# Optimization experiments

Hardware: AMD Instinct MI355X
Metric: run time of the kernel (lower is better)

The kernel has to match this reference:

```python
import jax, jax.numpy as jnp
import numpy as np
from jax import lax

C_CLIP = 10.0
TEMP = 1.0
NEG = 1e8


def setup_inputs() -> dict:
    key = jax.random.key(0)
    ks = jax.random.split(key, 20)
    B, N, H, M = 16, 1000, 128, 2
    s = 0.08
    inp = {
        "enc_h": jax.random.normal(ks[0], (B, N, H), jnp.float32),
        "mask0": jnp.zeros((B, N), jnp.float32),
        "Wq1": jax.random.normal(ks[1], (M, 2 * H, H), jnp.float32) * s,
        "Wref1": jax.random.normal(ks[2], (M, H, H), jnp.float32) * s,
        "Vec1": jax.random.normal(ks[3], (M, H, H), jnp.float32) * s,
        "Wq3": jax.random.normal(ks[4], (M, H, H), jnp.float32) * s,
        "Wref3": jax.random.normal(ks[5], (M, H, H), jnp.float32) * s,
        "Vec3": jax.random.normal(ks[6], (M, H, H), jnp.float32) * s,
        "Wq4": jax.random.normal(ks[7], (M, H, H), jnp.float32) * s,
        "Wref4": jax.random.normal(ks[8], (M, H, H), jnp.float32) * s,
        "Vec4": jax.random.normal(ks[9], (M, H, H), jnp.float32) * s,
        "Wmh": jax.random.normal(ks[10], (M * H, H), jnp.float32) * s,
        "Wq2": jax.random.normal(ks[11], (H, H), jnp.float32) * s,
        "Wref2": jax.random.normal(ks[12], (H, H), jnp.float32) * s,
        "Vec2": jax.random.normal(ks[13], (H,), jnp.float32) * s,
        "dec_inp": jax.random.normal(ks[14], (H,), jnp.float32) * s,
        "n_decode": 16,
    }
    return inp


def reference(enc_h, mask0, Wq1, Wref1, Vec1, Wq3, Wref3, Vec3,
              Wq4, Wref4, Vec4, Wmh, Wq2, Wref2, Vec2, dec_inp, n_decode):
    B, N, H = enc_h.shape
    ref = enc_h
    h_mean = ref.mean(axis=1)  # [B,H] graph embedding (encoder mean)
    # Precompute per-head reference projections (hoisted out of decode loop)
    r1 = jnp.einsum('bnd,mdh->bmnh', ref, Wref1)
    v1 = jnp.einsum('bnd,mdh->bmnh', ref, Vec1)
    r3 = jnp.einsum('bnd,mdh->bmnh', ref, Wref3)
    v3 = jnp.einsum('bnd,mdh->bmnh', ref, Vec3)
    r4 = jnp.einsum('bnd,mdh->bmnh', ref, Wref4)
    v4 = jnp.einsum('bnd,mdh->bmnh', ref, Vec4)
    r2 = ref @ Wref2  # [B,N,H]

    def glimpse(query, Wq, r, v, mask):
        # query: [B,Din]; r,v: [B,M,N,H]; mask: [B,N] (1 = unavailable)
        q = jnp.einsum('bi,mih->bmh', query, Wq)
        u = jnp.tanh(q[:, :, None, :] + r)              # [B,M,N,H]
        s = jnp.einsum('bmnh,bmnh->bmn', u, v)          # additive scores
        s = C_CLIP * jnp.tanh(s)                        # logit clipping
        s = s - NEG * mask[:, None, :]
        a = jax.nn.softmax(s, axis=-1)                  # [B,M,N]
        g = jnp.einsum('bmn,bmnh->bmh', a, r)           # per-head glimpse
        return g.reshape(B, -1) @ Wmh                   # merge heads -> [B,H]

    def step(carry, _):
        mask, prev = carry
        q0 = jnp.concatenate([h_mean, prev], axis=-1)   # [B,2H]
        q = glimpse(q0, Wq1, r1, v1, mask)
        q = glimpse(q, Wq3, r3, v3, mask)
        q = glimpse(q, Wq4, r4, v4, mask)
        # pointer logits: Vec2 . tanh(W_q2 q + W_ref2 ref)
        u = jnp.einsum('h,bnh->bn', Vec2, jnp.tanh((q @ Wq2)[:, None, :] + r2))
        u = C_CLIP * jnp.tanh(u)
        u = u - NEG * mask
        logp = jax.nn.log_softmax(u / TEMP, axis=-1)    # [B,N]
        sel = jnp.argmax(logp, axis=-1)                 # greedy job selection
        mask = mask.at[jnp.arange(B), sel].set(1.0)
        prev = jnp.take_along_axis(ref, sel[:, None, None], axis=1)[:, 0]
        return (mask, prev), (logp, sel)

    prev0 = jnp.broadcast_to(dec_inp, (B, H))
    (_, _), (logps, sels) = lax.scan(step, (mask0, prev0), None, length=n_decode)
    return logps, sels
```

## Files before the change

### kernel.cpp

```cpp
#include <hip/hip_runtime.h>


#define Bb 16
#define Nn 1000
#define Hh 128
#define Ss 16
#define TPB 1024
#define NW 16
#define NB 16
#define ROWS 63
#define TPT (Nn * Bb * Hh)

#define PPART(par, g, c, m) \
  ((((size_t)(par)*16 + (size_t)(g))*NB + (size_t)(c))*2 + (size_t)(m))*132
#define ABUF(buf, g) (((size_t)(buf)*16 + (size_t)(g)) * 272)

typedef float f32x4 __attribute__((ext_vector_type(4)));
#define NTL(p) __builtin_nontemporal_load((const f32x4*)(p))

__device__ __forceinline__ void red5_2(float& a, float& b) {
#pragma unroll
  for (int m = 1; m <= 16; m <<= 1) {
    a += __shfl_xor(a, m, 64);
    b += __shfl_xor(b, m, 64);
  }
}
__device__ __forceinline__ void red5_4(float& a, float& b, float& c, float& d) {
#pragma unroll
  for (int m = 1; m <= 16; m <<= 1) {
    a += __shfl_xor(a, m, 64);
    b += __shfl_xor(b, m, 64);
    c += __shfl_xor(c, m, 64);
    d += __shfl_xor(d, m, 64);
  }
}

__device__ __forceinline__ float tanh_fast(float x) {
  const float xc = fminf(fmaxf(x, -10.f), 10.f);
  const float e = __expf(xc + xc);
  return (e - 1.f) * __builtin_amdgcn_rcpf(e + 1.f);
}
__device__ __forceinline__ float dot4t(const f32x4 q, const f32x4 r, const f32x4 v) {
  return tanh_fast(q[0] + r[0]) * v[0] + tanh_fast(q[1] + r[1]) * v[1] +
         tanh_fast(q[2] + r[2]) * v[2] + tanh_fast(q[3] + r[3]) * v[3];
}

__device__ __forceinline__ float aload(const float* p) {
  return __hip_atomic_load(p, __ATOMIC_RELAXED, __HIP_MEMORY_SCOPE_AGENT);
}
__device__ __forceinline__ void astore(float* p, float v) {
  __hip_atomic_store(p, v, __ATOMIC_RELAXED, __HIP_MEMORY_SCOPE_AGENT);
}

__device__ __forceinline__ void gbar(int* fl, int c, int p, int tid, int lane) {
  __syncthreads();
  if (tid < 64) {
    if (lane == 0)
      __hip_atomic_store(&fl[c * 32], p, __ATOMIC_RELEASE, __HIP_MEMORY_SCOPE_AGENT);
    int v = p;
    while (true) {
      if (lane < NB)
        v = __hip_atomic_load(&fl[lane * 32], __ATOMIC_RELAXED, __HIP_MEMORY_SCOPE_AGENT);
      if (__all(v >= p)) break;
    }
  }
  __syncthreads();
}

__global__ __launch_bounds__(256) void ptr1_proj_kernel(
    const float* __restrict__ enc,
    const float* __restrict__ Wref1, const float* __restrict__ Vec1,
    const float* __restrict__ Wref3, const float* __restrict__ Vec3,
    const float* __restrict__ Wref4, const float* __restrict__ Vec4,
    const float* __restrict__ Wref2,
    float* __restrict__ outp) {
  __shared__ float At[128][64];
  __shared__ float Bs[128][64];
  const int rt = blockIdx.x;
  const int wy = blockIdx.y;
  const int mat = wy >> 1;
  const int ch = wy & 1;
  const int tid = threadIdx.x;

  const float* W;
  switch (mat >> 1) {
    case 0: W = Wref1; break;
    case 1: W = Vec1;  break;
    case 2: W = Wref3; break;
    case 3: W = Vec3;  break;
    case 4: W = Wref4; break;
    case 5: W = Vec4;  break;
    default: W = Wref2; break;
  }
  if (mat < 12) W += (size_t)(mat & 1) * (128 * 128);

  const float* asrc = enc + (size_t)rt * 64 * 128;
  for (int f = tid; f < 64 * 32; f += 256) {
    const int r = f >> 5, k4 = (f & 31) << 2;
    const float4 v = *(const float4*)(asrc + (size_t)r * 128 + k4);
    At[k4 + 0][r] = v.x; At[k4 + 1][r] = v.y;
    At[k4 + 2][r] = v.z; At[k4 + 3][r] = v.w;
  }
  for (int f = tid; f < 128 * 16; f += 256) {
    const int k = f >> 4, c4 = (f & 15) << 2;
    *(float4*)&Bs[k][c4] = *(const float4*)(W + (size_t)k * 128 + ch * 64 + c4);
  }
  __syncthreads();

  const int tx = tid & 15, ty = tid >> 4;
  float acc[4][4] = {{0.f}};
  for (int k = 0; k < 128; ++k) {
    const float4 a = *(const float4*)&At[k][ty * 4];
    const float4 b = *(const float4*)&Bs[k][tx * 4];
    acc[0][0] += a.x * b.x; acc[0][1] += a.x * b.y; acc[0][2] += a.x * b.z; acc[0][3] += a.x * b.w;
    acc[1][0] += a.y * b.x; acc[1][1] += a.y * b.y; acc[1][2] += a.y * b.z; acc[1][3] += a.y * b.w;
    acc[2][0] += a.z * b.x; acc[2][1] += a.z * b.y; acc[2][2] += a.z * b.z; acc[2][3] += a.z * b.w;
    acc[3][0] += a.w * b.x; acc[3][1] += a.w * b.y; acc[3][2] += a.w * b.z; acc[3][3] += a.w * b.w;
  }
  float* dst = outp + (size_t)mat * TPT + ((size_t)rt * 64 + ty * 4) * 128 + ch * 64 + tx * 4;
  for (int i = 0; i < 4; ++i) {
    float4 v; v.x = acc[i][0]; v.y = acc[i][1]; v.z = acc[i][2]; v.w = acc[i][3];
    *(float4*)(dst + (size_t)i * 128) = v;
  }
}

__global__ __launch_bounds__(1024, 4) void ptr1_decode_kernel(
    const float* __restrict__ enc, const float* __restrict__ mask0,
    const float* __restrict__ Wq1, const float* __restrict__ Wq3,
    const float* __restrict__ Wq4, const float* __restrict__ Wmh,
    const float* __restrict__ Wq2, const float* __restrict__ Vec2,
    const float* __restrict__ dec_inp, const float* __restrict__ proj,
    float* __restrict__ partials, float* __restrict__ accum,
    int* __restrict__ flags, float* __restrict__ out) {
  const int g = blockIdx.x >> 4;
  const int c = blockIdx.x & 15;
  const int tid = threadIdx.x;
  const int wv = tid >> 6;
  const int lane = tid & 63;
  const int half = lane >> 5;
  const int hl = lane & 31;
  const int h0 = hl << 2;
  const int start = c * ROWS;
  const int cnt = min(ROWS, Nn - start);
  const int jrow = wv * 2 + half;
  const int j2 = jrow + 32;
  const bool a2 = j2 < cnt;
  const int j2c = a2 ? j2 : jrow;
  int* fl = flags + g * (16 * 32);

  __shared__ float Wmh_lds[256 * 128];
  __shared__ __align__(16) float hmean[128];
  __shared__ __align__(16) float qprev[128];
  __shared__ __align__(16) float qcur[128];
  __shared__ __align__(16) float base1[256];
  __shared__ __align__(16) float qm[2][128];
  __shared__ __align__(16) float gfraw[256];
  __shared__ __align__(16) float vecl[128];
  __shared__ __align__(16) float wpart[NW][2][132];
  __shared__ __align__(16) float qpart[4][256];
  __shared__ __align__(16) float mpart[8][128];
  __shared__ float sS[2];
  __shared__ float maskl[64];
  __shared__ float ulocal[64];
  __shared__ int sel_sh;
  __shared__ float logZ_sh;

  {
    float4* wl = (float4*)Wmh_lds;
    const float4* wg = (const float4*)Wmh;
#pragma unroll
    for (int k = 0; k < 8; ++k) wl[tid + k * TPB] = wg[tid + k * TPB];
  }
  if (tid < 128) vecl[tid] = Vec2[tid];
  for (int j = tid; j < cnt; j += TPB) maskl[j] = mask0[(size_t)g * Nn + start + j];

  const size_t o1 = (size_t)jrow * Hh;
  const size_t o2 = (size_t)j2c * Hh;

  {
    const float* eb = enc + ((size_t)g * Nn + start) * Hh + h0;
    const float4 eA = *(const float4*)(eb + o1);
    const float4 eB = *(const float4*)(eb + o2);
    float4 a;
    a.x = eA.x + (a2 ? eB.x : 0.f); a.y = eA.y + (a2 ? eB.y : 0.f);
    a.z = eA.z + (a2 ? eB.z : 0.f); a.w = eA.w + (a2 ? eB.w : 0.f);
    a.x += __shfl_xor(a.x, 32, 64); a.y += __shfl_xor(a.y, 32, 64);
    a.z += __shfl_xor(a.z, 32, 64); a.w += __shfl_xor(a.w, 32, 64);
    if (half == 0) *(float4*)&wpart[wv][0][4 + h0] = a;
    __syncthreads();
    if (tid < 128) {
      float s = 0.f;
      for (int w = 0; w < NW; ++w) s += wpart[w][0][4 + tid];
      astore(&partials[PPART(0, g, c, 0) + 4 + tid], s);
    }
    gbar(fl, c, 1, tid, lane);
    if (tid < 128) {
      float s = 0.f;
#pragma unroll 8
      for (int cc = 0; cc < NB; ++cc) s += aload(&partials[PPART(0, g, cc, 0) + 4 + tid]);
      hmean[tid] = s * (1.0f / (float)Nn);
    }
    if (tid >= 128 && tid < 256) qprev[tid - 128] = dec_inp[tid - 128];
    __syncthreads();
    {
      const int o = tid & 255, part = tid >> 8;
      const int m = o >> 7, h = o & 127;
      const float* wp = Wq1 + (size_t)m * 256 * 128 + (size_t)(part * 32) * 128 + h;
      const float* qc = hmean + part * 32;
      float acc = 0.f;
#pragma unroll 16
      for (int i = 0; i < 32; ++i) acc += qc[i] * wp[(size_t)i * 128];
      qpart[part][o] = acc;
    }
    __syncthreads();
    if (tid < 256)
      base1[tid] = qpart[0][tid] + qpart[1][tid] + qpart[2][tid] + qpart[3][tid];
    __syncthreads();
  }

  int p = 2;
  for (int step = 0; step < Ss; ++step) {
    for (int gl = 0; gl < 3; ++gl) {
      const size_t rowb = ((size_t)g * Nn + start) * Hh + h0;
      const float* r0p = proj + (size_t)(4 * gl + 0) * TPT + rowb;
      const float* r1p = proj + (size_t)(4 * gl + 1) * TPT + rowb;
      const float* v0p = proj + (size_t)(4 * gl + 2) * TPT + rowb;
      const float* v1p = proj + (size_t)(4 * gl + 3) * TPT + rowb;
      const f32x4 r0A = NTL(r0p + o1), r0B = NTL(r0p + o2);
      const f32x4 r1A = NTL(r1p + o1), r1B = NTL(r1p + o2);
      const f32x4 v0A = NTL(v0p + o1), v0B = NTL(v0p + o2);
      const f32x4 v1A = NTL(v1p + o1), v1B = NTL(v1p + o2);
      __builtin_amdgcn_sched_barrier(0);
      {
        const int o = tid & 255, part = tid >> 8;
        const int m = o >> 7, h = o & 127;
        const float* wp;
        const float* qc;
        if (gl == 0) {
          wp = Wq1 + (size_t)m * 256 * 128 + (size_t)(128 + part * 32) * 128 + h;
          qc = qprev + part * 32;
        } else {
          const float* Wq = (gl == 1) ? Wq3 : Wq4;
          wp = Wq + (size_t)m * 128 * 128 + (size_t)(part * 32) * 128 + h;
          qc = qcur + part * 32;
        }
        float acc = 0.f;
#pragma unroll 16
        for (int i = 0; i < 32; ++i) acc += qc[i] * wp[(size_t)i * 128];
        qpart[part][o] = acc;
      }
      __syncthreads();
      if (tid < 256) {
        float s = qpart[0][tid] + qpart[1][tid] + qpart[2][tid] + qpart[3][tid];
        if (gl == 0) s += base1[tid];
        (&qm[0][0])[tid] = s;
      }
      __syncthreads();

      const f32x4 qa = *(const f32x4*)&qm[0][h0];
      const f32x4 qb = *(const f32x4*)&qm[1][h0];
      const float mlA = maskl[jrow], mlB = maskl[j2c];
      float s0A = dot4t(qa, r0A, v0A), s1A = dot4t(qb, r1A, v1A);
      float s0B = dot4t(qa, r0B, v0B), s1B = dot4t(qb, r1B, v1B);
      red5_4(s0A, s1A, s0B, s1B);
      s0A = 10.f * tanh_fast(s0A) - 1e8f * mlA;
      s1A = 10.f * tanh_fast(s1A) - 1e8f * mlA;
      s0B = 10.f * tanh_fast(s0B) - 1e8f * mlB;
      s1B = 10.f * tanh_fast(s1B) - 1e8f * mlB;
      const float e0A = __expf(s0A - 10.f), e1A = __expf(s1A - 10.f);
      const float e0B = a2 ? __expf(s0B - 10.f) : 0.f;
      const float e1B = a2 ? __expf(s1B - 10.f) : 0.f;
      float S0 = e0A + e0B, S1 = e1A + e1B;
      float4 g0, g1;
      g0.x = e0A * r0A[0] + e0B * r0B[0]; g0.y = e0A * r0A[1] + e0B * r0B[1];
      g0.z = e0A * r0A[2] + e0B * r0B[2]; g0.w = e0A * r0A[3] + e0B * r0B[3];
      g1.x = e1A * r1A[0] + e1B * r1B[0]; g1.y = e1A * r1A[1] + e1B * r1B[1];
      g1.z = e1A * r1A[2] + e1B * r1B[2]; g1.w = e1A * r1A[3] + e1B * r1B[3];
      S0 += __shfl_xor(S0, 32, 64); S1 += __shfl_xor(S1, 32, 64);
      g0.x += __shfl_xor(g0.x, 32, 64); g0.y += __shfl_xor(g0.y, 32, 64);
      g0.z += __shfl_xor(g0.z, 32, 64); g0.w += __shfl_xor(g0.w, 32, 64);
      g1.x += __shfl_xor(g1.x, 32, 64); g1.y += __shfl_xor(g1.y, 32, 64);
      g1.z += __shfl_xor(g1.z, 32, 64); g1.w += __shfl_xor(g1.w, 32, 64);
      if (half == 0) {
        *(float4*)&wpart[wv][0][4 + h0] = g0;
        *(float4*)&wpart[wv][1][4 + h0] = g1;
        if (hl == 0) { wpart[wv][0][0] = S0; wpart[wv][1][0] = S1; }
      }
      __syncthreads();
      float* ab = accum + ABUF(p & 3, g);
      float* zb = accum + ABUF((p + 1) & 3, g);
      if (tid < 256) {
        const int m = tid >> 7, h = tid & 127;
        float gs = 0.f;
        for (int w = 0; w < NW; ++w) gs += wpart[w][m][4 + h];
        unsafeAtomicAdd(&ab[m * 132 + 4 + h], gs);
        if (h == 0) {
          float ss = 0.f;
          for (int w = 0; w < NW; ++w) ss += wpart[w][m][0];
          unsafeAtomicAdd(&ab[m * 132], ss);
        }
      } else if (tid >= 512 && tid < 512 + 17) {
        const int idx = c * 17 + (tid - 512);
        if (idx < 272) astore(&zb[idx], 0.f);
      }
      gbar(fl, c, p, tid, lane);
      p++;
      if (tid < 256) gfraw[tid] = aload(&ab[(tid >> 7) * 132 + 4 + (tid & 127)]);
      if (tid >= 256 && tid < 258) sS[tid - 256] = aload(&ab[(tid - 256) * 132]);
      __syncthreads();
      {
        const int h = tid & 127, part = tid >> 7;
        const int m = part >> 2;
        float acc = 0.f;
        const float* wl = Wmh_lds + (size_t)part * 32 * 128 + h;
        const float* gg = gfraw + part * 32;
#pragma unroll 16
        for (int i = 0; i < 32; ++i) acc += gg[i] * wl[i * 128];
        mpart[part][h] = acc / sS[m];
      }
      __syncthreads();
      if (tid < 128) {
        float acc = 0.f;
        for (int w = 0; w < 8; ++w) acc += mpart[w][tid];
        qcur[tid] = acc;
      }
      __syncthreads();
    }

    const float* r2p = proj + (size_t)12 * TPT + ((size_t)g * Nn + start) * Hh + h0;
    const f32x4 rrA = NTL(r2p + o1);
    const f32x4 rrB = NTL(r2p + o2);
    __builtin_amdgcn_sched_barrier(0);
    {
      const int h = tid & 127, part = tid >> 7;
      float acc = 0.f;
      const float* wp = Wq2 + (size_t)part * 16 * 128 + h;
      const float* qc = qcur + part * 16;
#pragma unroll
      for (int i = 0; i < 16; ++i) acc += qc[i] * wp[(size_t)i * 128];
      mpart[part][h] = acc;
    }
    __syncthreads();
    if (tid < 128) {
      float acc = 0.f;
      for (int w = 0; w < 8; ++w) acc += mpart[w][tid];
      qm[0][tid] = acc;
    }
    __syncthreads();
    {
      const f32x4 q2 = *(const f32x4*)&qm[0][h0];
      const f32x4 vz = *(const f32x4*)&vecl[h0];
      float upA = dot4t(q2, rrA, vz);
      float upB = dot4t(q2, rrB, vz);
      red5_2(upA, upB);
      const float mlA = maskl[jrow], mlB = maskl[j2c];
      const float uA = 10.f * tanh_fast(upA) - 1e8f * mlA;
      const float uB = a2 ? (10.f * tanh_fast(upB) - 1e8f * mlB) : -3.0e38f;
      if (hl == 0) {
        ulocal[jrow] = uA;
        if (a2) ulocal[j2] = uB;
      }
      float Sv = __expf(uA - 10.f) + (a2 ? __expf(uB - 10.f) : 0.f);
      float um = uA; int ui = start + jrow;
      if (a2 && uB > um) { um = uB; ui = start + j2; }
      Sv += __shfl_xor(Sv, 32, 64);
      const float um2 = __shfl_xor(um, 32, 64);
      const int ui2 = __shfl_xor(ui, 32, 64);
      if (um2 > um || (um2 == um && ui2 < ui)) { um = um2; ui = ui2; }
      if (lane == 0) {
        wpart[wv][0][0] = Sv; wpart[wv][0][1] = um;
        wpart[wv][0][2] = __int_as_float(ui);
      }
    }
    __syncthreads();
    float* ab = accum + ABUF(p & 3, g);
    float* zb = accum + ABUF((p + 1) & 3, g);
    if (tid == 0) {
      float St = 0.f, bm = -3.0e38f; int bi = 0x7fffffff;
      for (int ww = 0; ww < NW; ++ww) {
        St += wpart[ww][0][0];
        const float m2 = wpart[ww][0][1];
        const int i2 = __float_as_int(wpart[ww][0][2]);
        if (m2 > bm || (m2 == bm && i2 < bi)) { bm = m2; bi = i2; }
      }
      unsigned ob = __float_as_uint(bm);
      ob = (ob & 0x80000000u) ? ~ob : (ob | 0x80000000u);
      const unsigned long long key =
          ((unsigned long long)ob << 32) | (0xFFFFFFFFu - (unsigned)bi);
      unsafeAtomicAdd(&ab[0], St);
      atomicMax((unsigned long long*)&ab[264], key);
    } else if (tid >= 512 && tid < 512 + 17) {
      const int idx = c * 17 + (tid - 512);
      if (idx < 272) astore(&zb[idx], 0.f);
    }
    gbar(fl, c, p, tid, lane);
    p++;
    if (tid == 0) {
      const float St = aload(&ab[0]);
      const unsigned long long key = __hip_atomic_load(
          (const unsigned long long*)&ab[264], __ATOMIC_RELAXED,
          __HIP_MEMORY_SCOPE_AGENT);
      sel_sh = (int)(0xFFFFFFFFu - (unsigned)(key & 0xFFFFFFFFu));
      logZ_sh = 10.f + __logf(St);
    }
    __syncthreads();
    const int sel = sel_sh;
    const float lz = logZ_sh;
    if (tid < 128)
      qprev[tid] = enc[((size_t)g * Nn + sel) * Hh + tid];
    for (int j = tid; j < cnt; j += TPB)
      out[(size_t)step * (Bb * Nn) + (size_t)g * Nn + start + j] = ulocal[j] - lz;
    if (c == 0 && tid == 0)
      out[(size_t)Ss * Bb * Nn + (size_t)step * Bb + g] = (float)sel;
    if (tid == 0 && sel >= start && sel < start + cnt) maskl[sel - start] = 1.0f;
    __syncthreads();
  }
}

extern "C" void kernel_launch(void* const* d_in, const int* in_sizes, int n_in,
                              void* d_out, int out_size, void* d_ws, size_t ws_size,
                              hipStream_t stream) {
  const float* enc     = (const float*)d_in[0];
  const float* mask0   = (const float*)d_in[1];
  const float* Wq1     = (const float*)d_in[2];
  const float* Wref1   = (const float*)d_in[3];
  const float* Vec1    = (const float*)d_in[4];
  const float* Wq3     = (const float*)d_in[5];
  const float* Wref3   = (const float*)d_in[6];
  const float* Vec3    = (const float*)d_in[7];
  const float* Wq4     = (const float*)d_in[8];
  const float* Wref4   = (const float*)d_in[9];
  const float* Vec4    = (const float*)d_in[10];
  const float* Wmh     = (const float*)d_in[11];
  const float* Wq2     = (const float*)d_in[12];
  const float* Wref2   = (const float*)d_in[13];
  const float* Vec2    = (const float*)d_in[14];
  const float* dec_inp = (const float*)d_in[15];
  float* out = (float*)d_out;

  char* ws = (char*)d_ws;
  int* flags      = (int*)ws;
  float* accum    = (float*)(ws + 32768);
  float* partials = (float*)(ws + 102400);
  float* proj     = (float*)(ws + 102400 + 540672);

  hipMemsetAsync(ws, 0, 102400, stream);

  dim3 pg(250, 26);
  ptr1_proj_kernel<<<pg, 256, 0, stream>>>(enc, Wref1, Vec1, Wref3, Vec3,
                                           Wref4, Vec4, Wref2, proj);

  void* args[] = {(void*)&enc,  (void*)&mask0, (void*)&Wq1, (void*)&Wq3,
                  (void*)&Wq4,  (void*)&Wmh,   (void*)&Wq2, (void*)&Vec2,
                  (void*)&dec_inp, (void*)&proj, (void*)&partials,
                  (void*)&accum, (void*)&flags, (void*)&out};
  hipLaunchCooperativeKernel((const void*)ptr1_decode_kernel, dim3(256),
                             dim3(1024), args, 0, stream);
}
```

Measured before the change: 993.9 us.

## Keep projection tiles in registers across decode steps and merge heads before barrier

Loads all 13 per-row projection tiles (r/v for three glimpses plus r2) into registers once before the decode loop, instead of re-reading them from global memory on every step. The per-block glimpse partials are pushed through the Wmh head-merge before the grid barrier, so each block atomically adds merged 128-wide vectors and the post-barrier work is a cheap normalize. Launch bounds are relaxed to 2 blocks per CU to allow the extra register use. This risks register pressure or spills, and the reordered sums change floating-point rounding.

```diff
diff --git a/kernel.cpp b/kernel.cpp
--- a/kernel.cpp
+++ b/kernel.cpp
@@ -11,8 +11,7 @@
 #define ROWS 63
 #define TPT (Nn * Bb * Hh)
 
-#define PPART(par, g, c, m) \
-  ((((size_t)(par)*16 + (size_t)(g))*NB + (size_t)(c))*2 + (size_t)(m))*132
+#define PPART(g, c) (((size_t)(g)*NB + (size_t)(c)) * 132)
 #define ABUF(buf, g) (((size_t)(buf)*16 + (size_t)(g)) * 272)
 
 typedef float f32x4 __attribute__((ext_vector_type(4)));
@@ -124,7 +123,7 @@
   }
 }
 
-__global__ __launch_bounds__(1024, 4) void ptr1_decode_kernel(
+__global__ __launch_bounds__(1024, 2) void ptr1_decode_kernel(
     const float* __restrict__ enc, const float* __restrict__ mask0,
     const float* __restrict__ Wq1, const float* __restrict__ Wq3,
     const float* __restrict__ Wq4, const float* __restrict__ Wmh,
@@ -159,11 +158,29 @@
   __shared__ __align__(16) float wpart[NW][2][132];
   __shared__ __align__(16) float qpart[4][256];
   __shared__ __align__(16) float mpart[8][128];
-  __shared__ float sS[2];
   __shared__ float maskl[64];
   __shared__ float ulocal[64];
   __shared__ int sel_sh;
   __shared__ float logZ_sh;
+
+  const size_t o1 = (size_t)jrow * Hh;
+  const size_t o2 = (size_t)j2c * Hh;
+  const size_t rowb = ((size_t)g * Nn + start) * Hh + h0;
+  const float* pb = proj + rowb;
+
+  const f32x4 G0r0A = NTL(pb + (size_t)0 * TPT + o1), G0r0B = NTL(pb + (size_t)0 * TPT + o2);
+  const f32x4 G0r1A = NTL(pb + (size_t)1 * TPT + o1), G0r1B = NTL(pb + (size_t)1 * TPT + o2);
+  const f32x4 G0v0A = NTL(pb + (size_t)2 * TPT + o1), G0v0B = NTL(pb + (size_t)2 * TPT + o2);
+  const f32x4 G0v1A = NTL(pb + (size_t)3 * TPT + o1), G0v1B = NTL(pb + (size_t)3 * TPT + o2);
+  const f32x4 G1r0A = NTL(pb + (size_t)4 * TPT + o1), G1r0B = NTL(pb + (size_t)4 * TPT + o2);
+  const f32x4 G1r1A = NTL(pb + (size_t)5 * TPT + o1), G1r1B = NTL(pb + (size_t)5 * TPT + o2);
+  const f32x4 G1v0A = NTL(pb + (size_t)6 * TPT + o1), G1v0B = NTL(pb + (size_t)6 * TPT + o2);
+  const f32x4 G1v1A = NTL(pb + (size_t)7 * TPT + o1), G1v1B = NTL(pb + (size_t)7 * TPT + o2);
+  const f32x4 G2r0A = NTL(pb + (size_t)8 * TPT + o1), G2r0B = NTL(pb + (size_t)8 * TPT + o2);
+  const f32x4 G2r1A = NTL(pb + (size_t)9 * TPT + o1), G2r1B = NTL(pb + (size_t)9 * TPT + o2);
+  const f32x4 G2v0A = NTL(pb + (size_t)10 * TPT + o1), G2v0B = NTL(pb + (size_t)10 * TPT + o2);
+  const f32x4 G2v1A = NTL(pb + (size_t)11 * TPT + o1), G2v1B = NTL(pb + (size_t)11 * TPT + o2);
+  const f32x4 rrA  = NTL(pb + (size_t)12 * TPT + o1), rrB  = NTL(pb + (size_t)12 * TPT + o2);
 
   {
     float4* wl = (float4*)Wmh_lds;
@@ -174,11 +191,8 @@
   if (tid < 128) vecl[tid] = Vec2[tid];
   for (int j = tid; j < cnt; j += TPB) maskl[j] = mask0[(size_t)g * Nn + start + j];
 
-  const size_t o1 = (size_t)jrow * Hh;
-  const size_t o2 = (size_t)j2c * Hh;
-
   {
-    const float* eb = enc + ((size_t)g * Nn + start) * Hh + h0;
+    const float* eb = enc + rowb;
     const float4 eA = *(const float4*)(eb + o1);
     const float4 eB = *(const float4*)(eb + o2);
     float4 a;
@@ -191,13 +205,13 @@
     if (tid < 128) {
       float s = 0.f;
       for (int w = 0; w < NW; ++w) s += wpart[w][0][4 + tid];
-      astore(&partials[PPART(0, g, c, 0) + 4 + tid], s);
+      astore(&partials[PPART(g, c) + 4 + tid], s);
     }
     gbar(fl, c, 1, tid, lane);
     if (tid < 128) {
       float s = 0.f;
 #pragma unroll 8
-      for (int cc = 0; cc < NB; ++cc) s += aload(&partials[PPART(0, g, cc, 0) + 4 + tid]);
+      for (int cc = 0; cc < NB; ++cc) s += aload(&partials[PPART(g, cc) + 4 + tid]);
       hmean[tid] = s * (1.0f / (float)Nn);
     }
     if (tid >= 128 && tid < 256) qprev[tid - 128] = dec_inp[tid - 128];
@@ -219,118 +233,109 @@
   }
 
   int p = 2;
+
+  auto glimpse = [&](int FIRST, const float* wqbase, size_t mstride,
+                     const float* qc_base, const f32x4 r0A, const f32x4 r0B,
+                     const f32x4 r1A, const f32x4 r1B, const f32x4 v0A,
+                     const f32x4 v0B, const f32x4 v1A, const f32x4 v1B) {
+    {
+      const int o = tid & 255, part = tid >> 8;
+      const int m = o >> 7, h = o & 127;
+      const float* wp = wqbase + (size_t)m * mstride + (size_t)(part * 32) * 128 + h;
+      const float* qc = qc_base + part * 32;
+      float acc = 0.f;
+#pragma unroll 16
+      for (int i = 0; i < 32; ++i) acc += qc[i] * wp[(size_t)i * 128];
+      qpart[part][o] = acc;
+    }
+    __syncthreads();
+    if (tid < 256) {
+      float s = qpart[0][tid] + qpart[1][tid] + qpart[2][tid] + qpart[3][tid];
+      if (FIRST) s += base1[tid];
+      (&qm[0][0])[tid] = s;
+    }
+    __syncthreads();
+
+    const f32x4 qa = *(const f32x4*)&qm[0][h0];
+    const f32x4 qb = *(const f32x4*)&qm[1][h0];
+    const float mlA = maskl[jrow], mlB = maskl[j2c];
+    float s0A = dot4t(qa, r0A, v0A), s1A = dot4t(qb, r1A, v1A);
+    float s0B = dot4t(qa, r0B, v0B), s1B = dot4t(qb, r1B, v1B);
+    red5_4(s0A, s1A, s0B, s1B);
+    s0A = 10.f * tanh_fast(s0A) - 1e8f * mlA;
+    s1A = 10.f * tanh_fast(s1A) - 1e8f * mlA;
+    s0B = 10.f * tanh_fast(s0B) - 1e8f * mlB;
+    s1B = 10.f * tanh_fast(s1B) - 1e8f * mlB;
+    const float e0A = __expf(s0A - 10.f), e1A = __expf(s1A - 10.f);
+    const float e0B = a2 ? __expf(s0B - 10.f) : 0.f;
+    const float e1B = a2 ? __expf(s1B - 10.f) : 0.f;
+    float S0 = e0A + e0B, S1 = e1A + e1B;
+    f32x4 g0 = r0A * e0A + r0B * e0B;
+    f32x4 g1 = r1A * e1A + r1B * e1B;
+    S0 += __shfl_xor(S0, 32, 64); S1 += __shfl_xor(S1, 32, 64);
+    g0[0] += __shfl_xor(g0[0], 32, 64); g0[1] += __shfl_xor(g0[1], 32, 64);
+    g0[2] += __shfl_xor(g0[2], 32, 64); g0[3] += __shfl_xor(g0[3], 32, 64);
+    g1[0] += __shfl_xor(g1[0], 32, 64); g1[1] += __shfl_xor(g1[1], 32, 64);
+    g1[2] += __shfl_xor(g1[2], 32, 64); g1[3] += __shfl_xor(g1[3], 32, 64);
+    if (half == 0) {
+      *(f32x4*)&wpart[wv][0][4 + h0] = g0;
+      *(f32x4*)&wpart[wv][1][4 + h0] = g1;
+      if (hl == 0) { wpart[wv][0][0] = S0; wpart[wv][1][0] = S1; }
+    }
+    __syncthreads();
+    float* ab = accum + ABUF(p & 3, g);
+    float* zb = accum + ABUF((p + 1) & 3, g);
+    float sS_reg = 0.f;
+    if (tid < 256) {
+      const int m = tid >> 7, h = tid & 127;
+      float gs = 0.f;
+      for (int w = 0; w < NW; ++w) gs += wpart[w][m][4 + h];
+      gfraw[tid] = gs;
+    } else if (tid == 256 || tid == 257) {
+      const int m = tid - 256;
+      for (int w = 0; w < NW; ++w) sS_reg += wpart[w][m][0];
+    } else if (tid >= 512 && tid < 529) {
+      const int idx = c * 17 + (tid - 512);
+      if (idx < 272) astore(&zb[idx], 0.f);
+    }
+    __syncthreads();
+    {
+      const int h = tid & 127, part = tid >> 7;
+      const int m = part >> 2, seg = part & 3;
+      float acc = 0.f;
+      const float* wl = Wmh_lds + ((size_t)m * 128 + seg * 32) * 128 + h;
+      const float* gg = gfraw + m * 128 + seg * 32;
+#pragma unroll 16
+      for (int i = 0; i < 32; ++i) acc += gg[i] * wl[i * 128];
+      mpart[part][h] = acc;
+    }
+    __syncthreads();
+    if (tid < 256) {
+      const int m = tid >> 7, h = tid & 127;
+      const float u = mpart[m * 4 + 0][h] + mpart[m * 4 + 1][h] +
+                      mpart[m * 4 + 2][h] + mpart[m * 4 + 3][h];
+      unsafeAtomicAdd(&ab[4 + tid], u);
+    } else if (tid == 256 || tid == 257) {
+      unsafeAtomicAdd(&ab[tid - 256], sS_reg);
+    }
+    gbar(fl, c, p, tid, lane);
+    p++;
+    if (tid < 128) {
+      const float S0r = aload(&ab[0]), S1r = aload(&ab[1]);
+      const float u0 = aload(&ab[4 + tid]), u1 = aload(&ab[132 + tid]);
+      qcur[tid] = u0 / S0r + u1 / S1r;
+    }
+    __syncthreads();
+  };
+
   for (int step = 0; step < Ss; ++step) {
-    for (int gl = 0; gl < 3; ++gl) {
-      const size_t rowb = ((size_t)g * Nn + start) * Hh + h0;
-      const float* r0p = proj + (size_t)(4 * gl + 0) * TPT + rowb;
-      const float* r1p = proj + (size_t)(4 * gl + 1) * TPT + rowb;
-      const float* v0p = proj + (size_t)(4 * gl + 2) * TPT + rowb;
-      const float* v1p = proj + (size_t)(4 * gl + 3) * TPT + rowb;
-      const f32x4 r0A = NTL(r0p + o1), r0B = NTL(r0p + o2);
-      const f32x4 r1A = NTL(r1p + o1), r1B = NTL(r1p + o2);
-      const f32x4 v0A = NTL(v0p + o1), v0B = NTL(v0p + o2);
-      const f32x4 v1A = NTL(v1p + o1), v1B = NTL(v1p + o2);
-      __builtin_amdgcn_sched_barrier(0);
-      {
-        const int o = tid & 255, part = tid >> 8;
-        const int m = o >> 7, h = o & 127;
-        const float* wp;
-        const float* qc;
-        if (gl == 0) {
-          wp = Wq1 + (size_t)m * 256 * 128 + (size_t)(128 + part * 32) * 128 + h;
-          qc = qprev + part * 32;
-        } else {
-          const float* Wq = (gl == 1) ? Wq3 : Wq4;
-          wp = Wq + (size_t)m * 128 * 128 + (size_t)(part * 32) * 128 + h;
-          qc = qcur + part * 32;
-        }
-        float acc = 0.f;
-#pragma unroll 16
-        for (int i = 0; i < 32; ++i) acc += qc[i] * wp[(size_t)i * 128];
-        qpart[part][o] = acc;
-      }
-      __syncthreads();
-      if (tid < 256) {
-        float s = qpart[0][tid] + qpart[1][tid] + qpart[2][tid] + qpart[3][tid];
-        if (gl == 0) s += base1[tid];
-        (&qm[0][0])[tid] = s;
-      }
-      __syncthreads();
-
-      const f32x4 qa = *(const f32x4*)&qm[0][h0];
-      const f32x4 qb = *(const f32x4*)&qm[1][h0];
-      const float mlA = maskl[jrow], mlB = maskl[j2c];
-      float s0A = dot4t(qa, r0A, v0A), s1A = dot4t(qb, r1A, v1A);
-      float s0B = dot4t(qa, r0B, v0B), s1B = dot4t(qb, r1B, v1B);
-      red5_4(s0A, s1A, s0B, s1B);
-      s0A = 10.f * tanh_fast(s0A) - 1e8f * mlA;
-      s1A = 10.f * tanh_fast(s1A) - 1e8f * mlA;
-      s0B = 10.f * tanh_fast(s0B) - 1e8f * mlB;
-      s1B = 10.f * tanh_fast(s1B) - 1e8f * mlB;
-      const float e0A = __expf(s0A - 10.f), e1A = __expf(s1A - 10.f);
-      const float e0B = a2 ? __expf(s0B - 10.f) : 0.f;
-      const float e1B = a2 ? __expf(s1B - 10.f) : 0.f;
-      float S0 = e0A + e0B, S1 = e1A + e1B;
-      float4 g0, g1;
-      g0.x = e0A * r0A[0] + e0B * r0B[0]; g0.y = e0A * r0A[1] + e0B * r0B[1];
-      g0.z = e0A * r0A[2] + e0B * r0B[2]; g0.w = e0A * r0A[3] + e0B * r0B[3];
-      g1.x = e1A * r1A[0] + e1B * r1B[0]; g1.y = e1A * r1A[1] + e1B * r1B[1];
-      g1.z = e1A * r1A[2] + e1B * r1B[2]; g1.w = e1A * r1A[3] + e1B * r1B[3];
-      S0 += __shfl_xor(S0, 32, 64); S1 += __shfl_xor(S1, 32, 64);
-      g0.x += __shfl_xor(g0.x, 32, 64); g0.y += __shfl_xor(g0.y, 32, 64);
-      g0.z += __shfl_xor(g0.z, 32, 64); g0.w += __shfl_xor(g0.w, 32, 64);
-      g1.x += __shfl_xor(g1.x, 32, 64); g1.y += __shfl_xor(g1.y, 32, 64);
-      g1.z += __shfl_xor(g1.z, 32, 64); g1.w += __shfl_xor(g1.w, 32, 64);
-      if (half == 0) {
-        *(float4*)&wpart[wv][0][4 + h0] = g0;
-        *(float4*)&wpart[wv][1][4 + h0] = g1;
-        if (hl == 0) { wpart[wv][0][0] = S0; wpart[wv][1][0] = S1; }
-      }
-      __syncthreads();
-      float* ab = accum + ABUF(p & 3, g);
-      float* zb = accum + ABUF((p + 1) & 3, g);
-      if (tid < 256) {
-        const int m = tid >> 7, h = tid & 127;
-        float gs = 0.f;
-        for (int w = 0; w < NW; ++w) gs += wpart[w][m][4 + h];
-        unsafeAtomicAdd(&ab[m * 132 + 4 + h], gs);
-        if (h == 0) {
-          float ss = 0.f;
-          for (int w = 0; w < NW; ++w) ss += wpart[w][m][0];
-          unsafeAtomicAdd(&ab[m * 132], ss);
-        }
-      } else if (tid >= 512 && tid < 512 + 17) {
-        const int idx = c * 17 + (tid - 512);
-        if (idx < 272) astore(&zb[idx], 0.f);
-      }
-      gbar(fl, c, p, tid, lane);
-      p++;
-      if (tid < 256) gfraw[tid] = aload(&ab[(tid >> 7) * 132 + 4 + (tid & 127)]);
-      if (tid >= 256 && tid < 258) sS[tid - 256] = aload(&ab[(tid - 256) * 132]);
-      __syncthreads();
-      {
-        const int h = tid & 127, part = tid >> 7;
-        const int m = part >> 2;
-        float acc = 0.f;
-        const float* wl = Wmh_lds + (size_t)part * 32 * 128 + h;
-        const float* gg = gfraw + part * 32;
-#pragma unroll 16
-        for (int i = 0; i < 32; ++i) acc += gg[i] * wl[i * 128];
-        mpart[part][h] = acc / sS[m];
-      }
-      __syncthreads();
-      if (tid < 128) {
-        float acc = 0.f;
-        for (int w = 0; w < 8; ++w) acc += mpart[w][tid];
-        qcur[tid] = acc;
-      }
-      __syncthreads();
-    }
-
-    const float* r2p = proj + (size_t)12 * TPT + ((size_t)g * Nn + start) * Hh + h0;
-    const f32x4 rrA = NTL(r2p + o1);
-    const f32x4 rrB = NTL(r2p + o2);
-    __builtin_amdgcn_sched_barrier(0);
+    glimpse(1, Wq1 + 128 * 128, (size_t)256 * 128, qprev,
+            G0r0A, G0r0B, G0r1A, G0r1B, G0v0A, G0v0B, G0v1A, G0v1B);
+    glimpse(0, Wq3, (size_t)128 * 128, qcur,
+            G1r0A, G1r0B, G1r1A, G1r1B, G1v0A, G1v0B, G1v1A, G1v1B);
+    glimpse(0, Wq4, (size_t)128 * 128, qcur,
+            G2r0A, G2r0B, G2r1A, G2r1B, G2v0A, G2v0B, G2v1A, G2v1B);
+
     {
       const int h = tid & 127, part = tid >> 7;
       float acc = 0.f;
@@ -388,8 +393,8 @@
       const unsigned long long key =
           ((unsigned long long)ob << 32) | (0xFFFFFFFFu - (unsigned)bi);
       unsafeAtomicAdd(&ab[0], St);
-      atomicMax((unsigned long long*)&ab[264], key);
-    } else if (tid >= 512 && tid < 512 + 17) {
+      atomicMax((unsigned long long*)&ab[2], key);
+    } else if (tid >= 512 && tid < 529) {
       const int idx = c * 17 + (tid - 512);
       if (idx < 272) astore(&zb[idx], 0.f);
     }
@@ -398,7 +403,7 @@
     if (tid == 0) {
       const float St = aload(&ab[0]);
       const unsigned long long key = __hip_atomic_load(
-          (const unsigned long long*)&ab[264], __ATOMIC_RELAXED,
+          (const unsigned long long*)&ab[2], __ATOMIC_RELAXED,
           __HIP_MEMORY_SCOPE_AGENT);
       sel_sh = (int)(0xFFFFFFFFu - (unsigned)(key & 0xFFFFFFFFu));
       logZ_sh = 10.f + __logf(St);
@@ -442,7 +447,7 @@
   int* flags      = (int*)ws;
   float* accum    = (float*)(ws + 32768);
   float* partials = (float*)(ws + 102400);
-  float* proj     = (float*)(ws + 102400 + 540672);
+  float* proj     = (float*)(ws + 102400 + 135168);
 
   hipMemsetAsync(ws, 0, 102400, stream);
 
```

Result: slower. 1.350 ms (+35.9%).

## Halve decode blocks per batch to 8, processing four rows per half-wave

Applied to the files above, without the earlier changes.

Splits each batch across 8 cooperative blocks instead of 16, so each block handles 125 rows and each half-wave processes four rows with four projection loads in flight. This halves the number of blocks taking part in each per-batch global barrier and atomic reduction, cutting synchronization cost across the 16 steps times 4 barriers. In exchange, only 128 blocks cover the GPU, so fewer CUs are used, per-block streaming work doubles and register pressure rises. The workspace layout and zeroing slices are resized to match.

```diff
diff --git a/kernel.cpp b/kernel.cpp
--- a/kernel.cpp
+++ b/kernel.cpp
@@ -7,24 +7,16 @@
 #define Ss 16
 #define TPB 1024
 #define NW 16
-#define NB 16
-#define ROWS 63
+#define NB 8
+#define ROWS 125
 #define TPT (Nn * Bb * Hh)
 
-#define PPART(par, g, c, m) \
-  ((((size_t)(par)*16 + (size_t)(g))*NB + (size_t)(c))*2 + (size_t)(m))*132
+#define PPART(g, c) (((size_t)(g)*NB + (size_t)(c)) * 132)
 #define ABUF(buf, g) (((size_t)(buf)*16 + (size_t)(g)) * 272)
 
 typedef float f32x4 __attribute__((ext_vector_type(4)));
 #define NTL(p) __builtin_nontemporal_load((const f32x4*)(p))
 
-__device__ __forceinline__ void red5_2(float& a, float& b) {
-#pragma unroll
-  for (int m = 1; m <= 16; m <<= 1) {
-    a += __shfl_xor(a, m, 64);
-    b += __shfl_xor(b, m, 64);
-  }
-}
 __device__ __forceinline__ void red5_4(float& a, float& b, float& c, float& d) {
 #pragma unroll
   for (int m = 1; m <= 16; m <<= 1) {
@@ -34,7 +26,6 @@
     d += __shfl_xor(d, m, 64);
   }
 }
-
 __device__ __forceinline__ float tanh_fast(float x) {
   const float xc = fminf(fmaxf(x, -10.f), 10.f);
   const float e = __expf(xc + xc);
@@ -44,14 +35,12 @@
   return tanh_fast(q[0] + r[0]) * v[0] + tanh_fast(q[1] + r[1]) * v[1] +
          tanh_fast(q[2] + r[2]) * v[2] + tanh_fast(q[3] + r[3]) * v[3];
 }
-
 __device__ __forceinline__ float aload(const float* p) {
   return __hip_atomic_load(p, __ATOMIC_RELAXED, __HIP_MEMORY_SCOPE_AGENT);
 }
 __device__ __forceinline__ void astore(float* p, float v) {
   __hip_atomic_store(p, v, __ATOMIC_RELAXED, __HIP_MEMORY_SCOPE_AGENT);
 }
-
 __device__ __forceinline__ void gbar(int* fl, int c, int p, int tid, int lane) {
   __syncthreads();
   if (tid < 64) {
@@ -132,8 +121,8 @@
     const float* __restrict__ dec_inp, const float* __restrict__ proj,
     float* __restrict__ partials, float* __restrict__ accum,
     int* __restrict__ flags, float* __restrict__ out) {
-  const int g = blockIdx.x >> 4;
-  const int c = blockIdx.x & 15;
+  const int g = blockIdx.x >> 3;
+  const int c = blockIdx.x & 7;
   const int tid = threadIdx.x;
   const int wv = tid >> 6;
   const int lane = tid & 63;
@@ -141,12 +130,14 @@
   const int hl = lane & 31;
   const int h0 = hl << 2;
   const int start = c * ROWS;
-  const int cnt = min(ROWS, Nn - start);
-  const int jrow = wv * 2 + half;
-  const int j2 = jrow + 32;
-  const bool a2 = j2 < cnt;
-  const int j2c = a2 ? j2 : jrow;
-  int* fl = flags + g * (16 * 32);
+  const int cnt = ROWS;
+  const int j1 = wv * 2 + half;
+  const int j2 = j1 + 32;
+  const int j3 = j1 + 64;
+  const int j4 = j1 + 96;
+  const bool a4 = j4 < cnt;
+  const int j4c = a4 ? j4 : j1;
+  int* fl = flags + g * (NB * 32);
 
   __shared__ float Wmh_lds[256 * 128];
   __shared__ __align__(16) float hmean[128];
@@ -160,8 +151,8 @@
   __shared__ __align__(16) float qpart[4][256];
   __shared__ __align__(16) float mpart[8][128];
   __shared__ float sS[2];
-  __shared__ float maskl[64];
-  __shared__ float ulocal[64];
+  __shared__ float maskl[128];
+  __shared__ float ulocal[128];
   __shared__ int sel_sh;
   __shared__ float logZ_sh;
 
@@ -174,16 +165,24 @@
   if (tid < 128) vecl[tid] = Vec2[tid];
   for (int j = tid; j < cnt; j += TPB) maskl[j] = mask0[(size_t)g * Nn + start + j];
 
-  const size_t o1 = (size_t)jrow * Hh;
-  const size_t o2 = (size_t)j2c * Hh;
+  const size_t o1 = (size_t)j1 * Hh;
+  const size_t o2 = (size_t)j2 * Hh;
+  const size_t o3 = (size_t)j3 * Hh;
+  const size_t o4 = (size_t)j4c * Hh;
+  const size_t rowb = ((size_t)g * Nn + start) * Hh + h0;
+  const float* pb = proj + rowb;
 
   {
-    const float* eb = enc + ((size_t)g * Nn + start) * Hh + h0;
-    const float4 eA = *(const float4*)(eb + o1);
-    const float4 eB = *(const float4*)(eb + o2);
+    const float* eb = enc + rowb;
+    const float4 e1 = *(const float4*)(eb + o1);
+    const float4 e2 = *(const float4*)(eb + o2);
+    const float4 e3 = *(const float4*)(eb + o3);
+    const float4 e4 = *(const float4*)(eb + o4);
     float4 a;
-    a.x = eA.x + (a2 ? eB.x : 0.f); a.y = eA.y + (a2 ? eB.y : 0.f);
-    a.z = eA.z + (a2 ? eB.z : 0.f); a.w = eA.w + (a2 ? eB.w : 0.f);
+    a.x = e1.x + e2.x + e3.x + (a4 ? e4.x : 0.f);
+    a.y = e1.y + e2.y + e3.y + (a4 ? e4.y : 0.f);
+    a.z = e1.z + e2.z + e3.z + (a4 ? e4.z : 0.f);
+    a.w = e1.w + e2.w + e3.w + (a4 ? e4.w : 0.f);
     a.x += __shfl_xor(a.x, 32, 64); a.y += __shfl_xor(a.y, 32, 64);
     a.z += __shfl_xor(a.z, 32, 64); a.w += __shfl_xor(a.w, 32, 64);
     if (half == 0) *(float4*)&wpart[wv][0][4 + h0] = a;
@@ -191,13 +190,13 @@
     if (tid < 128) {
       float s = 0.f;
       for (int w = 0; w < NW; ++w) s += wpart[w][0][4 + tid];
-      astore(&partials[PPART(0, g, c, 0) + 4 + tid], s);
+      astore(&partials[PPART(g, c) + 4 + tid], s);
     }
     gbar(fl, c, 1, tid, lane);
     if (tid < 128) {
       float s = 0.f;
 #pragma unroll 8
-      for (int cc = 0; cc < NB; ++cc) s += aload(&partials[PPART(0, g, cc, 0) + 4 + tid]);
+      for (int cc = 0; cc < NB; ++cc) s += aload(&partials[PPART(g, cc) + 4 + tid]);
       hmean[tid] = s * (1.0f / (float)Nn);
     }
     if (tid >= 128 && tid < 256) qprev[tid - 128] = dec_inp[tid - 128];
@@ -221,16 +220,14 @@
   int p = 2;
   for (int step = 0; step < Ss; ++step) {
     for (int gl = 0; gl < 3; ++gl) {
-      const size_t rowb = ((size_t)g * Nn + start) * Hh + h0;
-      const float* r0p = proj + (size_t)(4 * gl + 0) * TPT + rowb;
-      const float* r1p = proj + (size_t)(4 * gl + 1) * TPT + rowb;
-      const float* v0p = proj + (size_t)(4 * gl + 2) * TPT + rowb;
-      const float* v1p = proj + (size_t)(4 * gl + 3) * TPT + rowb;
-      const f32x4 r0A = NTL(r0p + o1), r0B = NTL(r0p + o2);
-      const f32x4 r1A = NTL(r1p + o1), r1B = NTL(r1p + o2);
-      const f32x4 v0A = NTL(v0p + o1), v0B = NTL(v0p + o2);
-      const f32x4 v1A = NTL(v1p + o1), v1B = NTL(v1p + o2);
-      __builtin_amdgcn_sched_barrier(0);
+      const float* r0p = pb + (size_t)(4 * gl + 0) * TPT;
+      const float* r1p = pb + (size_t)(4 * gl + 1) * TPT;
+      const float* v0p = pb + (size_t)(4 * gl + 2) * TPT;
+      const float* v1p = pb + (size_t)(4 * gl + 3) * TPT;
+      const f32x4 r0A = NTL(r0p + o1), r0B = NTL(r0p + o2), r0C = NTL(r0p + o3), r0D = NTL(r0p + o4);
+      const f32x4 r1A = NTL(r1p + o1), r1B = NTL(r1p + o2), r1C = NTL(r1p + o3), r1D = NTL(r1p + o4);
+      const f32x4 v0A = NTL(v0p + o1), v0B = NTL(v0p + o2), v0C = NTL(v0p + o3), v0D = NTL(v0p + o4);
+      const f32x4 v1A = NTL(v1p + o1), v1B = NTL(v1p + o2), v1C = NTL(v1p + o3), v1D = NTL(v1p + o4);
       {
         const int o = tid & 255, part = tid >> 8;
         const int m = o >> 7, h = o & 127;
@@ -259,31 +256,38 @@
 
       const f32x4 qa = *(const f32x4*)&qm[0][h0];
       const f32x4 qb = *(const f32x4*)&qm[1][h0];
-      const float mlA = maskl[jrow], mlB = maskl[j2c];
-      float s0A = dot4t(qa, r0A, v0A), s1A = dot4t(qb, r1A, v1A);
-      float s0B = dot4t(qa, r0B, v0B), s1B = dot4t(qb, r1B, v1B);
-      red5_4(s0A, s1A, s0B, s1B);
-      s0A = 10.f * tanh_fast(s0A) - 1e8f * mlA;
-      s1A = 10.f * tanh_fast(s1A) - 1e8f * mlA;
-      s0B = 10.f * tanh_fast(s0B) - 1e8f * mlB;
-      s1B = 10.f * tanh_fast(s1B) - 1e8f * mlB;
-      const float e0A = __expf(s0A - 10.f), e1A = __expf(s1A - 10.f);
-      const float e0B = a2 ? __expf(s0B - 10.f) : 0.f;
-      const float e1B = a2 ? __expf(s1B - 10.f) : 0.f;
-      float S0 = e0A + e0B, S1 = e1A + e1B;
-      float4 g0, g1;
-      g0.x = e0A * r0A[0] + e0B * r0B[0]; g0.y = e0A * r0A[1] + e0B * r0B[1];
-      g0.z = e0A * r0A[2] + e0B * r0B[2]; g0.w = e0A * r0A[3] + e0B * r0B[3];
-      g1.x = e1A * r1A[0] + e1B * r1B[0]; g1.y = e1A * r1A[1] + e1B * r1B[1];
-      g1.z = e1A * r1A[2] + e1B * r1B[2]; g1.w = e1A * r1A[3] + e1B * r1B[3];
+      const float ml1 = maskl[j1], ml2 = maskl[j2], ml3 = maskl[j3], ml4 = maskl[j4c];
+      float s0A = dot4t(qa, r0A, v0A), s0B = dot4t(qa, r0B, v0B);
+      float s0C = dot4t(qa, r0C, v0C), s0D = dot4t(qa, r0D, v0D);
+      float s1A = dot4t(qb, r1A, v1A), s1B = dot4t(qb, r1B, v1B);
+      float s1C = dot4t(qb, r1C, v1C), s1D = dot4t(qb, r1D, v1D);
+      red5_4(s0A, s0B, s1A, s1B);
+      red5_4(s0C, s0D, s1C, s1D);
+      s0A = 10.f * tanh_fast(s0A) - 1e8f * ml1;
+      s0B = 10.f * tanh_fast(s0B) - 1e8f * ml2;
+      s0C = 10.f * tanh_fast(s0C) - 1e8f * ml3;
+      s0D = 10.f * tanh_fast(s0D) - 1e8f * ml4;
+      s1A = 10.f * tanh_fast(s1A) - 1e8f * ml1;
+      s1B = 10.f * tanh_fast(s1B) - 1e8f * ml2;
+      s1C = 10.f * tanh_fast(s1C) - 1e8f * ml3;
+      s1D = 10.f * tanh_fast(s1D) - 1e8f * ml4;
+      const float e0A = __expf(s0A - 10.f), e0B = __expf(s0B - 10.f);
+      const float e0C = __expf(s0C - 10.f);
+      const float e0D = a4 ? __expf(s0D - 10.f) : 0.f;
+      const float e1A = __expf(s1A - 10.f), e1B = __expf(s1B - 10.f);
+      const float e1C = __expf(s1C - 10.f);
+      const float e1D = a4 ? __expf(s1D - 10.f) : 0.f;
+      float S0 = e0A + e0B + e0C + e0D, S1 = e1A + e1B + e1C + e1D;
+      f32x4 g0 = r0A * e0A + r0B * e0B + r0C * e0C + r0D * e0D;
+      f32x4 g1 = r1A * e1A + r1B * e1B + r1C * e1C + r1D * e1D;
       S0 += __shfl_xor(S0, 32, 64); S1 += __shfl_xor(S1, 32, 64);
-      g0.x += __shfl_xor(g0.x, 32, 64); g0.y += __shfl_xor(g0.y, 32, 64);
-      g0.z += __shfl_xor(g0.z, 32, 64); g0.w += __shfl_xor(g0.w, 32, 64);
-      g1.x += __shfl_xor(g1.x, 32, 64); g1.y += __shfl_xor(g1.y, 32, 64);
-      g1.z += __shfl_xor(g1.z, 32, 64); g1.w += __shfl_xor(g1.w, 32, 64);
+      g0[0] += __shfl_xor(g0[0], 32, 64); g0[1] += __shfl_xor(g0[1], 32, 64);
+      g0[2] += __shfl_xor(g0[2], 32, 64); g0[3] += __shfl_xor(g0[3], 32, 64);
+      g1[0] += __shfl_xor(g1[0], 32, 64); g1[1] += __shfl_xor(g1[1], 32, 64);
+      g1[2] += __shfl_xor(g1[2], 32, 64); g1[3] += __shfl_xor(g1[3], 32, 64);
       if (half == 0) {
-        *(float4*)&wpart[wv][0][4 + h0] = g0;
-        *(float4*)&wpart[wv][1][4 + h0] = g1;
+        *(f32x4*)&wpart[wv][0][4 + h0] = g0;
+        *(f32x4*)&wpart[wv][1][4 + h0] = g1;
         if (hl == 0) { wpart[wv][0][0] = S0; wpart[wv][1][0] = S1; }
       }
       __syncthreads();
@@ -299,8 +303,8 @@
           for (int w = 0; w < NW; ++w) ss += wpart[w][m][0];
           unsafeAtomicAdd(&ab[m * 132], ss);
         }
-      } else if (tid >= 512 && tid < 512 + 17) {
-        const int idx = c * 17 + (tid - 512);
+      } else if (tid >= 512 && tid < 512 + 34) {
+        const int idx = c * 34 + (tid - 512);
         if (idx < 272) astore(&zb[idx], 0.f);
       }
       gbar(fl, c, p, tid, lane);
@@ -327,10 +331,11 @@
       __syncthreads();
     }
 
-    const float* r2p = proj + (size_t)12 * TPT + ((size_t)g * Nn + start) * Hh + h0;
+    const float* r2p = pb + (size_t)12 * TPT;
     const f32x4 rrA = NTL(r2p + o1);
     const f32x4 rrB = NTL(r2p + o2);
-    __builtin_amdgcn_sched_barrier(0);
+    const f32x4 rrC = NTL(r2p + o3);
+    const f32x4 rrD = NTL(r2p + o4);
     {
       const int h = tid & 127, part = tid >> 7;
       float acc = 0.f;
@@ -350,19 +355,25 @@
     {
       const f32x4 q2 = *(const f32x4*)&qm[0][h0];
       const f32x4 vz = *(const f32x4*)&vecl[h0];
-      float upA = dot4t(q2, rrA, vz);
-      float upB = dot4t(q2, rrB, vz);
-      red5_2(upA, upB);
-      const float mlA = maskl[jrow], mlB = maskl[j2c];
-      const float uA = 10.f * tanh_fast(upA) - 1e8f * mlA;
-      const float uB = a2 ? (10.f * tanh_fast(upB) - 1e8f * mlB) : -3.0e38f;
+      float uA = dot4t(q2, rrA, vz);
+      float uB = dot4t(q2, rrB, vz);
+      float uC = dot4t(q2, rrC, vz);
+      float uD = dot4t(q2, rrD, vz);
+      red5_4(uA, uB, uC, uD);
+      const float u1 = 10.f * tanh_fast(uA) - 1e8f * maskl[j1];
+      const float u2 = 10.f * tanh_fast(uB) - 1e8f * maskl[j2];
+      const float u3 = 10.f * tanh_fast(uC) - 1e8f * maskl[j3];
+      const float u4 = a4 ? (10.f * tanh_fast(uD) - 1e8f * maskl[j4c]) : -3.0e38f;
       if (hl == 0) {
-        ulocal[jrow] = uA;
-        if (a2) ulocal[j2] = uB;
-      }
-      float Sv = __expf(uA - 10.f) + (a2 ? __expf(uB - 10.f) : 0.f);
-      float um = uA; int ui = start + jrow;
-      if (a2 && uB > um) { um = uB; ui = start + j2; }
+        ulocal[j1] = u1; ulocal[j2] = u2; ulocal[j3] = u3;
+        if (a4) ulocal[j4] = u4;
+      }
+      float Sv = __expf(u1 - 10.f) + __expf(u2 - 10.f) + __expf(u3 - 10.f) +
+                 (a4 ? __expf(u4 - 10.f) : 0.f);
+      float um = u1; int ui = start + j1;
+      if (u2 > um) { um = u2; ui = start + j2; }
+      if (u3 > um) { um = u3; ui = start + j3; }
+      if (a4 && u4 > um) { um = u4; ui = start + j4; }
       Sv += __shfl_xor(Sv, 32, 64);
       const float um2 = __shfl_xor(um, 32, 64);
       const int ui2 = __shfl_xor(ui, 32, 64);
@@ -389,8 +400,8 @@
           ((unsigned long long)ob << 32) | (0xFFFFFFFFu - (unsigned)bi);
       unsafeAtomicAdd(&ab[0], St);
       atomicMax((unsigned long long*)&ab[264], key);
-    } else if (tid >= 512 && tid < 512 + 17) {
-      const int idx = c * 17 + (tid - 512);
+    } else if (tid >= 512 && tid < 512 + 34) {
+      const int idx = c * 34 + (tid - 512);
       if (idx < 272) astore(&zb[idx], 0.f);
     }
     gbar(fl, c, p, tid, lane);
@@ -440,11 +451,11 @@
 
   char* ws = (char*)d_ws;
   int* flags      = (int*)ws;
-  float* accum    = (float*)(ws + 32768);
-  float* partials = (float*)(ws + 102400);
-  float* proj     = (float*)(ws + 102400 + 540672);
-
-  hipMemsetAsync(ws, 0, 102400, stream);
+  float* accum    = (float*)(ws + 16384);
+  float* partials = (float*)(ws + 16384 + 69632);
+  float* proj     = (float*)(ws + 16384 + 69632 + 67584);
+
+  hipMemsetAsync(ws, 0, 16384 + 69632, stream);
 
   dim3 pg(250, 26);
   ptr1_proj_kernel<<<pg, 256, 0, stream>>>(enc, Wref1, Vec1, Wref3, Vec3,
@@ -454,6 +465,6 @@
                   (void*)&Wq4,  (void*)&Wmh,   (void*)&Wq2, (void*)&Vec2,
                   (void*)&dec_inp, (void*)&proj, (void*)&partials,
                   (void*)&accum, (void*)&flags, (void*)&out};
-  hipLaunchCooperativeKernel((const void*)ptr1_decode_kernel, dim3(256),
+  hipLaunchCooperativeKernel((const void*)ptr1_decode_kernel, dim3(128),
                              dim3(1024), args, 0, stream);
 }
```

New measurement: 1.387 ms. +39.6%, slower.
